# Kernel optimization log

Hardware: AMD Instinct MI355X
Metric: run time of the kernel (lower is better)

## Reference

```python
import jax, jax.numpy as jnp
import numpy as np

# Axial permutations for num_dimensions=3, emb_dim=-1 (total rank 5), att_dims=[1,2,3]
PERMS = [[0, 2, 3, 1, 4], [0, 1, 3, 2, 4], [0, 1, 2, 3, 4]]
H_SELF = 8
H_CROSS = 8
E_HEAD = 64  # dims_embed[0] / (num_heads_self + num_heads_cross) = 1024/16


def layernorm(x, eps=1e-5):
    # nn.LayerNorm(elementwise_affine=False)
    m = x.mean(axis=-1, keepdims=True)
    v = x.var(axis=-1, keepdims=True)
    return (x - m) * jax.lax.rsqrt(v + eps)


def cross_attention(x, kv, wq, wkv, h, e):
    # x: [bb, t, d_q], kv: [bb, t_kv, d_kv]
    q = x @ wq                                   # [bb, t, h*e]
    k, v = jnp.split(kv @ wkv, 2, axis=-1)       # each [bb, t_kv, h*e]
    bb, t = q.shape[0], q.shape[1]
    tk = k.shape[1]
    q = q.reshape(bb, t, h, e)
    k = k.reshape(bb, tk, h, e)
    v = v.reshape(bb, tk, h, e)
    dots = jnp.einsum('bihe,bjhe->bhij', q, k) * (e ** -0.5)
    attn = jax.nn.softmax(dots, axis=-1)
    out = jnp.einsum('bhij,bjhe->bihe', attn, v)
    return out.reshape(bb, t, h * e)


def permute_to_from(x, kv, perm, wq, wkv, h, e):
    inv = list(np.argsort(perm))
    ax = jnp.transpose(x, perm)
    axkv = jnp.transpose(kv, perm)
    shape = list(ax.shape)
    shape_kv = list(axkv.shape)
    t, d = shape[-2], shape[-1]
    t_kv, d_kv = shape_kv[-2], shape_kv[-1]
    r1 = shape[1] / shape_kv[1]
    r2 = shape[2] / shape_kv[2]
    if int(r1) != 1:
        axkv = jnp.repeat(axkv, max(1, int(r1)), axis=1)
        ax = jnp.repeat(ax, max(1, int(1.0 / r1)), axis=1)
    if int(r2) != 1:
        axkv = jnp.repeat(axkv, max(1, int(r2)), axis=2)
        ax = jnp.repeat(ax, max(1, int(1.0 / r2)), axis=2)
    assert ax.shape[1:3] == axkv.shape[1:3]
    perm_shape = list(ax.shape)
    out = cross_attention(ax.reshape(-1, t, d), axkv.reshape(-1, t_kv, d_kv), wq, wkv, h, e)
    out = out.reshape(perm_shape[:-1] + [-1])
    if shape[1] < shape_kv[1]:  # field0 coarser along perm dim 1 -> mean-pool back
        out = out.reshape(shape[:2] + [int(1.0 / r1)] + perm_shape[2:-1] + [-1]).mean(axis=2)
    if shape[2] < shape_kv[2]:
        out = out.reshape(shape[:3] + [int(1.0 / r2)] + perm_shape[3:-1] + [-1]).mean(axis=3)
    out = out.reshape(shape[:-1] + [-1])
    return jnp.transpose(out, inv)


def setup_inputs() -> dict:
    key = jax.random.key(0)
    ks = jax.random.split(key, 8)
    B, T, LA, LO, D0, D1 = 32, 12, 12, 12, 1024, 512
    s = 0.02
    return {
        'x0': jax.random.normal(ks[0], (B, T, LA, LO, D0), dtype=jnp.float32),
        'x1': jax.random.normal(ks[1], (B, T, LA // 2, LO // 2, D1), dtype=jnp.float32),
        'wq_self': jax.random.normal(ks[2], (3, D0, 512), dtype=jnp.float32) * s,
        'wkv_self': jax.random.normal(ks[3], (3, D0, 1024), dtype=jnp.float32) * s,
        'wq_cross': jax.random.normal(ks[4], (3, D0, 512), dtype=jnp.float32) * s,
        'wkv_cross': jax.random.normal(ks[5], (3, D1, 1024), dtype=jnp.float32) * s,
        'w_out': jax.random.normal(ks[6], (3, 1024, D0), dtype=jnp.float32) * s,
        'b_out': jnp.zeros((3, D0), dtype=jnp.float32),
    }


def reference(x0, x1, wq_self, wkv_self, wq_cross, wkv_cross, w_out, b_out):
    pass_through = x0
    f0 = layernorm(x0)
    f1 = layernorm(x1)
    for ip, perm in enumerate(PERMS):
        o_self = permute_to_from(f0, f0, perm, wq_self[ip], wkv_self[ip], H_SELF, E_HEAD)
        o_cross = permute_to_from(f0, f1, perm, wq_cross[ip], wkv_cross[ip], H_CROSS, E_HEAD)
        f0 = jnp.concatenate([o_self, o_cross], axis=-1) @ w_out[ip] + b_out[ip]
    return pass_through + f0
```

## Files before the change

### kernel.cpp

```cpp
#include <hip/hip_runtime.h>
#include <hip/hip_bf16.h>


typedef __bf16 bf16x8 __attribute__((ext_vector_type(8)));
typedef float floatx4 __attribute__((ext_vector_type(4)));

#define N0 55296
#define N1 13824

#define RAW_BARRIER() asm volatile("s_barrier" ::: "memory")
#define VMCNT(n) asm volatile("s_waitcnt vmcnt(" #n ")" ::: "memory")
#define SCHED_FENCE() __builtin_amdgcn_sched_barrier(0)

__device__ __forceinline__ void gload16(const void* g, void* l) {
    __builtin_amdgcn_global_load_lds(
        (const __attribute__((address_space(1))) unsigned int*)g,
        (__attribute__((address_space(3))) unsigned int*)l, 16, 0, 0);
}

template <int SIG>
__device__ __forceinline__ int mapRow(int i) {
    if (SIG == 0) return i;
    const int b = i / 1728, r = i % 1728;
    const int d1 = r / 144, r2 = r % 144, d2 = r2 / 12, d3 = r2 % 12;
    if (SIG == 1) return b * 1728 + d3 * 144 + d1 * 12 + d2;
    if (SIG == 2) return b * 1728 + d3 * 144 + d2 * 12 + d1;
    return b * 1728 + d1 * 144 + d3 * 12 + d2;
}

template <int D>
__device__ __forceinline__ void ln_body(const float* __restrict__ xr,
                                        __hip_bfloat16* __restrict__ yr)
{
    constexpr int V = D / 256;
    const int tid = threadIdx.x;
    float vals[V];
    if constexpr (V == 4) {
        const float4 t4 = *(const float4*)(xr + tid * 4);
        vals[0] = t4.x; vals[1] = t4.y; vals[2] = t4.z; vals[3] = t4.w;
    } else {
        const float2 t2 = *(const float2*)(xr + tid * 2);
        vals[0] = t2.x; vals[1] = t2.y;
    }
    float s = 0.f, q = 0.f;
#pragma unroll
    for (int k = 0; k < V; ++k) { s += vals[k]; q += vals[k] * vals[k]; }
#pragma unroll
    for (int off = 32; off > 0; off >>= 1) {
        s += __shfl_xor(s, off);
        q += __shfl_xor(q, off);
    }
    __shared__ float rs[4], rq[4];
    const int w = tid >> 6;
    if ((tid & 63) == 0) { rs[w] = s; rq[w] = q; }
    __syncthreads();
    s = rs[0] + rs[1] + rs[2] + rs[3];
    q = rq[0] + rq[1] + rq[2] + rq[3];
    const float mean = s * (1.f / D);
    const float var  = q * (1.f / D) - mean * mean;
    const float rstd = rsqrtf(var + 1e-5f);
    __hip_bfloat16 o[V];
#pragma unroll
    for (int k = 0; k < V; ++k) o[k] = __float2bfloat16((vals[k] - mean) * rstd);
    if constexpr (V == 4) *(uint2*)(yr + tid * 4) = *(const uint2*)o;
    else                  *(uint*)(yr + tid * 2)  = *(const uint*)o;
}

__global__ __launch_bounds__(256)
void ln_all(const float* __restrict__ x0, const float* __restrict__ x1,
            __hip_bfloat16* __restrict__ f0, __hip_bfloat16* __restrict__ f1)
{
    const int row = blockIdx.x;
    if (row < N0) {
        ln_body<1024>(x0 + (size_t)row * 1024, f0 + (size_t)row * 1024);
    } else {
        const int r = row - N0;
        ln_body<512>(x1 + (size_t)r * 512, f1 + (size_t)r * 512);
    }
}

__global__ __launch_bounds__(256)
void transpose_all(const float* __restrict__ wqs, const float* __restrict__ wkvs,
                   const float* __restrict__ wqc, const float* __restrict__ wkvc,
                   const float* __restrict__ wo,
                   __hip_bfloat16* __restrict__ W1t,
                   __hip_bfloat16* __restrict__ W2t,
                   __hip_bfloat16* __restrict__ W3t,
                   __hip_bfloat16* __restrict__ W3o)
{
    int idx = blockIdx.x;
    if (idx >= 8704) {
        const size_t i = ((size_t)(idx - 8704) * 256 + threadIdx.x) * 4;
        const float4 v = *(const float4*)(wo + i);
        __hip_bfloat16 o[4] = { __float2bfloat16(v.x), __float2bfloat16(v.y),
                                __float2bfloat16(v.z), __float2bfloat16(v.w) };
        *(uint2*)(W3o + i) = *(const uint2*)o;
        return;
    }
    const float* src;
    __hip_bfloat16* dst;
    int K, N;
    if (idx < 1536) {
        const int ip = idx / 512; idx %= 512; K = 1024; N = 512;
        src = wqs + (size_t)ip * 524288;  dst = W1t + (size_t)ip * 2097152;
    } else if (idx < 4608) {
        idx -= 1536;
        const int ip = idx / 1024; idx %= 1024; K = 1024; N = 1024;
        src = wkvs + (size_t)ip * 1048576; dst = W1t + (size_t)ip * 2097152 + 524288;
    } else if (idx < 6144) {
        idx -= 4608;
        const int ip = idx / 512; idx %= 512; K = 1024; N = 512;
        src = wqc + (size_t)ip * 524288;  dst = W1t + (size_t)ip * 2097152 + 1572864;
    } else if (idx < 7680) {
        idx -= 6144;
        const int ip = idx / 512; idx %= 512; K = 512; N = 1024;
        src = wkvc + (size_t)ip * 524288; dst = W2t + (size_t)ip * 524288;
    } else {
        idx -= 7680;
        K = 1024; N = 1024;
        src = wo + (size_t)2 * 1048576;  dst = W3t + (size_t)2 * 1048576;
    }
    const int tiles_x = N >> 5;
    const int n0 = (idx % tiles_x) * 32, k0 = (idx / tiles_x) * 32;

    __shared__ float tile[32][33];
    const int tx = threadIdx.x & 31, ty = threadIdx.x >> 5;
#pragma unroll
    for (int d = 0; d < 4; ++d)
        tile[ty + d * 8][tx] = src[(size_t)(k0 + ty + d * 8) * N + n0 + tx];
    __syncthreads();
#pragma unroll
    for (int d = 0; d < 4; ++d)
        dst[(size_t)(n0 + ty + d * 8) * K + k0 + tx] = __float2bfloat16(tile[tx][ty + d * 8]);
}

__global__ __launch_bounds__(256)
void bfold_kernel(const float* __restrict__ b_out,
                  const __hip_bfloat16* __restrict__ W1t,
                  float* __restrict__ bf)
{
    const int idx = blockIdx.x * 256 + threadIdx.x;
    const int j = idx >> 11, n = idx & 2047;
    const float* b = b_out + j * 1024;
    const __hip_bfloat16* w = W1t + ((size_t)(j + 1) * 2048 + n) * 1024;
    float s = 0.f;
#pragma unroll 4
    for (int d = 0; d < 1024; ++d) s += b[d] * __bfloat162float(w[d]);
    bf[idx] = s;
}

template <int EPI, int SIG>
__global__ __launch_bounds__(512)
void gemm8p(const __hip_bfloat16* __restrict__ A,
            const __hip_bfloat16* __restrict__ Bt,
            void* __restrict__ Cv,
            const float* __restrict__ bias,
            const float* __restrict__ resid,
            int M, int N, int K, int lda,
            size_t zsA, size_t zsB, size_t zsC)
{
    __shared__ __align__(16) char lds[131072];

    A  += (size_t)blockIdx.z * zsA;
    Bt += (size_t)blockIdx.z * zsB;
    Cv = (void*)((__hip_bfloat16*)Cv + (size_t)blockIdx.z * zsC);

    const int gx  = gridDim.x;
    const int nwg = gx * gridDim.y;
    const int bid = blockIdx.y * gx + blockIdx.x;
    const int swz = (bid & 7) * (nwg >> 3) + (bid >> 3);
    const int m0 = (swz / gx) * 256;
    const int n0 = (swz % gx) * 256;

    const int t    = threadIdx.x;
    const int w    = t >> 6;
    const int lane = t & 63;
    const int wr   = w >> 2;
    const int wc   = w & 3;
    const int fr   = lane & 15;
    const int ksl  = lane >> 4;

    floatx4 acc[8][4] = {};

    const int tr   = t >> 3;
    const int scol = ((t & 7) ^ (tr & 7)) << 3;
    const __hip_bfloat16* aP[4];
#pragma unroll
    for (int r = 0; r < 4; ++r)
        aP[r] = A + (size_t)mapRow<SIG>(m0 + tr + r * 64) * lda + scol;
    const __hip_bfloat16* bG = Bt + (size_t)(n0 + ((tr >> 5) * 64) + (tr & 31)) * K + scol;
    const int ldst = t * 16;

    const int cg0 = ksl ^ (fr & 7);
    const int aO0 = (wr * 64 + fr) * 128 + cg0 * 16;
    const int bO0 = (wc * 32 + fr) * 128 + cg0 * 16;

    auto stageA = [&](char* buf, int h, int ka) {
        gload16(aP[h]     + ka, buf + h * 16384 + ldst);
        gload16(aP[h + 2] + ka, buf + h * 16384 + 8192 + ldst);
    };
    auto stageB = [&](char* buf, int h, int kb) {
        gload16(bG + kb + (size_t)(h * 32)       * K, buf + 32768 + h * 16384 + ldst);
        gload16(bG + kb + (size_t)(h * 32 + 128) * K, buf + 32768 + h * 16384 + 8192 + ldst);
    };

    const char* bufC = lds;
    auto ldA = [&](int h, bf16x8 (&a)[2][4]) {
#pragma unroll
        for (int mm = 0; mm < 4; ++mm) {
            a[0][mm] = *(const bf16x8*)(bufC + h * 16384 + mm * 2048 + aO0);
            a[1][mm] = *(const bf16x8*)(bufC + h * 16384 + mm * 2048 + (aO0 ^ 64));
        }
    };
    auto ldB = [&](int h, bf16x8 (&b)[2][2]) {
#pragma unroll
        for (int nn = 0; nn < 2; ++nn) {
            b[0][nn] = *(const bf16x8*)(bufC + 32768 + h * 16384 + nn * 2048 + bO0);
            b[1][nn] = *(const bf16x8*)(bufC + 32768 + h * 16384 + nn * 2048 + (bO0 ^ 64));
        }
    };
    auto quad = [&](bf16x8 (&a)[2][4], bf16x8 (&b)[2][2], int mlo, int nlo) {
        __builtin_amdgcn_s_setprio(1);
#pragma unroll
        for (int kk = 0; kk < 2; ++kk)
#pragma unroll
            for (int mm = 0; mm < 4; ++mm)
#pragma unroll
                for (int nn = 0; nn < 2; ++nn)
                    acc[mlo + mm][nlo + nn] = __builtin_amdgcn_mfma_f32_16x16x32_bf16(
                        a[kk][mm], b[kk][nn], acc[mlo + mm][nlo + nn], 0, 0, 0);
        __builtin_amdgcn_s_setprio(0);
    };

    const int NT = K >> 6;

    stageA(lds, 0, 0);
    stageB(lds, 0, 0);
    stageA(lds, 1, 0);
    stageB(lds, 1, 0);
    VMCNT(4);
    RAW_BARRIER();

    bf16x8 a0[2][4], a1[2][4], b0[2][2], b1[2][2];
    ldA(0, a0);

    for (int tt = 0; tt < NT - 1; ++tt) {
        bufC = lds + ((tt & 1) << 16);
        char* bufN = lds + (((tt + 1) & 1) << 16);
        const int kc = (tt + 1) << 6;
        ldB(0, b0);
        stageA(bufN, 0, kc);
        SCHED_FENCE();
        quad(a0, b0, 0, 0);
        VMCNT(4); RAW_BARRIER();
        ldA(1, a1);
        stageB(bufN, 0, kc);
        SCHED_FENCE();
        quad(a1, b0, 4, 0);
        VMCNT(4); RAW_BARRIER();
        ldB(1, b1);
        stageA(bufN, 1, kc);
        SCHED_FENCE();
        quad(a0, b1, 0, 2);
        VMCNT(4); RAW_BARRIER();
        bufC = bufN;
        ldA(0, a0);
        stageB(bufN, 1, kc);
        SCHED_FENCE();
        quad(a1, b1, 4, 2);
        VMCNT(4); RAW_BARRIER();
    }

    bufC = lds + (((NT - 1) & 1) << 16);
    ldB(0, b0);
    SCHED_FENCE();
    quad(a0, b0, 0, 0);
    VMCNT(2); RAW_BARRIER();
    ldA(1, a1);
    SCHED_FENCE();
    quad(a1, b0, 4, 0);
    VMCNT(0); RAW_BARRIER();
    ldB(1, b1);
    SCHED_FENCE();
    quad(a0, b1, 0, 2);
    quad(a1, b1, 4, 2);

#pragma unroll
    for (int m = 0; m < 8; ++m) {
#pragma unroll
        for (int n = 0; n < 4; ++n) {
            const int col = n0 + wc * 64 + n * 16 + fr;
#pragma unroll
            for (int r = 0; r < 4; ++r) {
                const int row = m0 + wr * 128 + m * 16 + ksl * 4 + r;
                const size_t idx = (size_t)row * N + col;
                const float v = acc[m][n][r];
                if (EPI == 0) {
                    ((__hip_bfloat16*)Cv)[idx] = __float2bfloat16(v);
                } else if (EPI == 1) {
                    ((__hip_bfloat16*)Cv)[idx] = __float2bfloat16(v + bias[col]);
                } else {
                    ((float*)Cv)[idx] = resid[idx] + v + bias[col];
                }
            }
        }
    }
}

__global__ __launch_bounds__(512)
void attn_fused(const __hip_bfloat16* __restrict__ qkv,
                const __hip_bfloat16* __restrict__ kvc,
                __hip_bfloat16* __restrict__ out, int ip)
{
    __shared__ __align__(16) __hip_bfloat16 R[12][2056];
    __shared__ __align__(16) __hip_bfloat16 KV[12][1032];
    __shared__ __hip_bfloat16 P[16][12][12];

    const int g   = blockIdx.x;
    const int tid = threadIdx.x;

    const int b  = g / 144;
    const int u1 = (g / 12) % 12;
    const int u2 = g % 12;
    int kvb, kvstride, tkc;
    if (ip == 0) {
        kvb = b * 432 + (u1 >> 1) * 6 + (u2 >> 1); kvstride = 36; tkc = 12;
    } else if (ip == 1) {
        kvb = b * 432 + u1 * 36 + (u2 >> 1); kvstride = 6; tkc = 6;
    } else {
        kvb = b * 432 + u1 * 36 + (u2 >> 1) * 6; kvstride = 1; tkc = 6;
    }

    const uint4* src = (const uint4*)(qkv + (size_t)g * 12 * 2048);
    for (int idx = tid; idx < 12 * 256; idx += 512) {
        const int row = idx >> 8, cg = idx & 255;
        *(uint4*)(&R[row][cg * 8]) = src[row * 256 + cg];
    }
    for (int idx = tid; idx < tkc * 128; idx += 512) {
        const int row = idx >> 7, cg = idx & 127;
        const uint4* kvr = (const uint4*)(kvc + (size_t)(kvb + row * kvstride) * 3072);
        *(uint4*)(&KV[row][cg * 8]) = kvr[cg];
    }
    __syncthreads();

    const int nd_self = 8 * 12 * 12;
    const int nd = nd_self + 8 * 12 * tkc;
    for (int idx = tid; idx < nd; idx += 512) {
        int h, i, j;
        const bf16x8 *q8, *k8;
        const bool self = idx < nd_self;
        if (self) {
            h = idx / 144; const int rem = idx % 144; i = rem / 12; j = rem % 12;
            q8 = (const bf16x8*)(&R[i][h * 64]);
            k8 = (const bf16x8*)(&R[j][512 + h * 64]);
        } else {
            const int x = idx - nd_self;
            h = x / (12 * tkc); const int rem = x % (12 * tkc); i = rem / tkc; j = rem % tkc;
            q8 = (const bf16x8*)(&R[i][1536 + h * 64]);
            k8 = (const bf16x8*)(&KV[j][h * 64]);
        }
        float s = 0.f;
#pragma unroll
        for (int e = 0; e < 8; ++e) {
            const bf16x8 qv = q8[e];
            const bf16x8 kv = k8[e];
#pragma unroll
            for (int x2 = 0; x2 < 8; ++x2)
                s += (float)qv[x2] * (float)kv[x2];
        }
        P[self ? h : 8 + h][i][j] = __float2bfloat16(s * 0.125f);
    }
    __syncthreads();

    if (tid < 192) {
        const int half = tid / 96, h = (tid % 96) / 12, i = tid % 12;
        const int tk = half ? tkc : 12;
        __hip_bfloat16* p = &P[half * 8 + h][i][0];
        float v[12];
        float mx = -1e30f;
        for (int j = 0; j < tk; ++j) { v[j] = __bfloat162float(p[j]); mx = fmaxf(mx, v[j]); }
        float sum = 0.f;
        for (int j = 0; j < tk; ++j) { v[j] = __expf(v[j] - mx); sum += v[j]; }
        const float inv = 1.f / sum;
        for (int j = 0; j < tk; ++j) p[j] = __float2bfloat16(v[j] * inv);
    }
    __syncthreads();

    for (int idx = tid; idx < 12 * 128; idx += 512) {
        const int i = idx >> 7, g8 = idx & 127;
        float acc8[8] = {};
        int colbase;
        if (g8 < 64) {
            const int h = g8 >> 3;
            colbase = g8 * 8;
#pragma unroll
            for (int j = 0; j < 12; ++j) {
                const float p = __bfloat162float(P[h][i][j]);
                const bf16x8 v = *(const bf16x8*)(&R[j][1024 + g8 * 8]);
#pragma unroll
                for (int e = 0; e < 8; ++e) acc8[e] += p * (float)v[e];
            }
        } else {
            const int cc = g8 - 64;
            const int h = cc >> 3;
            colbase = 512 + cc * 8;
            for (int j = 0; j < tkc; ++j) {
                const float p = __bfloat162float(P[8 + h][i][j]);
                const bf16x8 v = *(const bf16x8*)(&KV[j][512 + cc * 8]);
#pragma unroll
                for (int e = 0; e < 8; ++e) acc8[e] += p * (float)v[e];
            }
        }
        __hip_bfloat16 o[8];
#pragma unroll
        for (int e = 0; e < 8; ++e) o[e] = __float2bfloat16(acc8[e]);
        *(uint4*)(out + (size_t)(g * 12 + i) * 1024 + colbase) = *(const uint4*)o;
    }
}

extern "C" void kernel_launch(void* const* d_in, const int* in_sizes, int n_in,
                              void* d_out, int out_size, void* d_ws, size_t ws_size,
                              hipStream_t stream)
{
    (void)in_sizes; (void)n_in; (void)out_size; (void)ws_size;
    const float* x0        = (const float*)d_in[0];
    const float* x1        = (const float*)d_in[1];
    const float* wq_self   = (const float*)d_in[2];
    const float* wkv_self  = (const float*)d_in[3];
    const float* wq_cross  = (const float*)d_in[4];
    const float* wkv_cross = (const float*)d_in[5];
    const float* w_out     = (const float*)d_in[6];
    const float* b_out     = (const float*)d_in[7];

    __hip_bfloat16* qkv = (__hip_bfloat16*)d_out;

    char* ws = (char*)d_ws;
    size_t off = 0;
    auto alloc = [&](size_t bytes) {
        void* p = ws + off;
        off += (bytes + 255) & ~(size_t)255;
        return p;
    };
    __hip_bfloat16* f0   = (__hip_bfloat16*)alloc((size_t)N0 * 1024 * 2);
    __hip_bfloat16* f1   = (__hip_bfloat16*)alloc((size_t)N1 * 512 * 2);
    __hip_bfloat16* kvc3 = (__hip_bfloat16*)alloc((size_t)N1 * 3072 * 2);
    __hip_bfloat16* W1t  = (__hip_bfloat16*)alloc((size_t)3 * 2048 * 1024 * 2);
    __hip_bfloat16* W2t  = (__hip_bfloat16*)alloc((size_t)3 * 1024 * 512 * 2);
    __hip_bfloat16* W3t  = (__hip_bfloat16*)alloc((size_t)3 * 1024 * 1024 * 2);
    __hip_bfloat16* W3o  = (__hip_bfloat16*)alloc((size_t)2 * 1024 * 1024 * 2);
    __hip_bfloat16* Wf   = (__hip_bfloat16*)alloc((size_t)2 * 2048 * 1024 * 2);
    float*          bfo  = (float*)alloc((size_t)2 * 2048 * 4);

    ln_all<<<N0 + N1, 256, 0, stream>>>(x0, x1, f0, f1);
    transpose_all<<<10752, 256, 0, stream>>>(wq_self, wkv_self, wq_cross,
                                             wkv_cross, w_out, W1t, W2t, W3t, W3o);
    bfold_kernel<<<16, 256, 0, stream>>>(b_out, W1t, bfo);
    gemm8p<0, 0><<<dim3(4, 8, 2), 512, 0, stream>>>(
        W1t + (size_t)2048 * 1024, W3o, Wf, nullptr, nullptr,
        2048, 1024, 1024, 1024,
        (size_t)2048 * 1024, (size_t)1024 * 1024, (size_t)2048 * 1024);
    gemm8p<0, 0><<<dim3(12, 54), 512, 0, stream>>>(
        f1, W2t, kvc3, nullptr, nullptr, N1, 3072, 512, 512, 0, 0, 0);

    gemm8p<0, 1><<<dim3(8, 216), 512, 0, stream>>>(
        f0, W1t, qkv, nullptr, nullptr, N0, 2048, 1024, 1024, 0, 0, 0);
    attn_fused<<<4608, 512, 0, stream>>>(qkv, kvc3, f0, 0);

    gemm8p<1, 2><<<dim3(8, 216), 512, 0, stream>>>(
        f0, Wf, qkv, bfo, nullptr, N0, 2048, 1024, 1024, 0, 0, 0);
    attn_fused<<<4608, 512, 0, stream>>>(qkv, kvc3 + 1024, f0, 1);

    gemm8p<1, 3><<<dim3(8, 216), 512, 0, stream>>>(
        f0, Wf + (size_t)2048 * 1024, qkv, bfo + 2048, nullptr, N0, 2048, 1024, 1024, 0, 0, 0);
    attn_fused<<<4608, 512, 0, stream>>>(qkv, kvc3 + 2048, f0, 2);

    gemm8p<2, 0><<<dim3(4, 216), 512, 0, stream>>>(
        f0, W3t + (size_t)2 * 1024 * 1024, d_out, b_out + 2 * 1024, x0,
        N0, 1024, 1024, 1024, 0, 0, 0);
}
```

Measured before the change: 1.452 ms.

## Replace double-buffered pipelined GEMM main loop with single-buffer synchronous loop

Removes the two-buffer software pipeline that overlapped global-to-LDS loads for the next K tile with MFMA work on the current one. Each iteration now loads the whole tile, waits for all loads to finish, computes, then waits on LDS reads before the next iteration. This halves shared memory to 64KB, which could allow more resident workgroups, but it exposes global memory latency on every K step.

```diff
diff --git a/kernel.cpp b/kernel.cpp
--- a/kernel.cpp
+++ b/kernel.cpp
@@ -10,7 +10,7 @@
 
 #define RAW_BARRIER() asm volatile("s_barrier" ::: "memory")
 #define VMCNT(n) asm volatile("s_waitcnt vmcnt(" #n ")" ::: "memory")
-#define SCHED_FENCE() __builtin_amdgcn_sched_barrier(0)
+#define LGKMCNT0() asm volatile("s_waitcnt lgkmcnt(0)" ::: "memory")
 
 __device__ __forceinline__ void gload16(const void* g, void* l) {
     __builtin_amdgcn_global_load_lds(
@@ -159,7 +159,7 @@
             int M, int N, int K, int lda,
             size_t zsA, size_t zsB, size_t zsC)
 {
-    __shared__ __align__(16) char lds[131072];
+    __shared__ __align__(16) char lds[65536];
 
     A  += (size_t)blockIdx.z * zsA;
     Bt += (size_t)blockIdx.z * zsB;
@@ -195,28 +195,27 @@
     const int aO0 = (wr * 64 + fr) * 128 + cg0 * 16;
     const int bO0 = (wc * 32 + fr) * 128 + cg0 * 16;
 
-    auto stageA = [&](char* buf, int h, int ka) {
-        gload16(aP[h]     + ka, buf + h * 16384 + ldst);
-        gload16(aP[h + 2] + ka, buf + h * 16384 + 8192 + ldst);
-    };
-    auto stageB = [&](char* buf, int h, int kb) {
-        gload16(bG + kb + (size_t)(h * 32)       * K, buf + 32768 + h * 16384 + ldst);
-        gload16(bG + kb + (size_t)(h * 32 + 128) * K, buf + 32768 + h * 16384 + 8192 + ldst);
-    };
-
-    const char* bufC = lds;
+    auto stageA = [&](int h, int ka) {
+        gload16(aP[h]     + ka, lds + h * 16384 + ldst);
+        gload16(aP[h + 2] + ka, lds + h * 16384 + 8192 + ldst);
+    };
+    auto stageB = [&](int h, int kb) {
+        gload16(bG + kb + (size_t)(h * 32)       * K, lds + 32768 + h * 16384 + ldst);
+        gload16(bG + kb + (size_t)(h * 32 + 128) * K, lds + 32768 + h * 16384 + 8192 + ldst);
+    };
+
     auto ldA = [&](int h, bf16x8 (&a)[2][4]) {
 #pragma unroll
         for (int mm = 0; mm < 4; ++mm) {
-            a[0][mm] = *(const bf16x8*)(bufC + h * 16384 + mm * 2048 + aO0);
-            a[1][mm] = *(const bf16x8*)(bufC + h * 16384 + mm * 2048 + (aO0 ^ 64));
+            a[0][mm] = *(const bf16x8*)(lds + h * 16384 + mm * 2048 + aO0);
+            a[1][mm] = *(const bf16x8*)(lds + h * 16384 + mm * 2048 + (aO0 ^ 64));
         }
     };
     auto ldB = [&](int h, bf16x8 (&b)[2][2]) {
 #pragma unroll
         for (int nn = 0; nn < 2; ++nn) {
-            b[0][nn] = *(const bf16x8*)(bufC + 32768 + h * 16384 + nn * 2048 + bO0);
-            b[1][nn] = *(const bf16x8*)(bufC + 32768 + h * 16384 + nn * 2048 + (bO0 ^ 64));
+            b[0][nn] = *(const bf16x8*)(lds + 32768 + h * 16384 + nn * 2048 + bO0);
+            b[1][nn] = *(const bf16x8*)(lds + 32768 + h * 16384 + nn * 2048 + (bO0 ^ 64));
         }
     };
     auto quad = [&](bf16x8 (&a)[2][4], bf16x8 (&b)[2][2], int mlo, int nlo) {
@@ -233,57 +232,25 @@
     };
 
     const int NT = K >> 6;
-
-    stageA(lds, 0, 0);
-    stageB(lds, 0, 0);
-    stageA(lds, 1, 0);
-    stageB(lds, 1, 0);
-    VMCNT(4);
-    RAW_BARRIER();
-
     bf16x8 a0[2][4], a1[2][4], b0[2][2], b1[2][2];
-    ldA(0, a0);
-
-    for (int tt = 0; tt < NT - 1; ++tt) {
-        bufC = lds + ((tt & 1) << 16);
-        char* bufN = lds + (((tt + 1) & 1) << 16);
-        const int kc = (tt + 1) << 6;
-        ldB(0, b0);
-        stageA(bufN, 0, kc);
-        SCHED_FENCE();
+
+    for (int tt = 0; tt < NT; ++tt) {
+        const int kc = tt << 6;
+        stageA(0, kc);
+        stageB(0, kc);
+        stageA(1, kc);
+        stageB(1, kc);
+        VMCNT(0); RAW_BARRIER();
+        ldA(0, a0); ldB(0, b0);
         quad(a0, b0, 0, 0);
-        VMCNT(4); RAW_BARRIER();
         ldA(1, a1);
-        stageB(bufN, 0, kc);
-        SCHED_FENCE();
         quad(a1, b0, 4, 0);
-        VMCNT(4); RAW_BARRIER();
         ldB(1, b1);
-        stageA(bufN, 1, kc);
-        SCHED_FENCE();
         quad(a0, b1, 0, 2);
-        VMCNT(4); RAW_BARRIER();
-        bufC = bufN;
-        ldA(0, a0);
-        stageB(bufN, 1, kc);
-        SCHED_FENCE();
         quad(a1, b1, 4, 2);
-        VMCNT(4); RAW_BARRIER();
-    }
-
-    bufC = lds + (((NT - 1) & 1) << 16);
-    ldB(0, b0);
-    SCHED_FENCE();
-    quad(a0, b0, 0, 0);
-    VMCNT(2); RAW_BARRIER();
-    ldA(1, a1);
-    SCHED_FENCE();
-    quad(a1, b0, 4, 0);
-    VMCNT(0); RAW_BARRIER();
-    ldB(1, b1);
-    SCHED_FENCE();
-    quad(a0, b1, 0, 2);
-    quad(a1, b1, 4, 2);
+        LGKMCNT0();
+        RAW_BARRIER();
+    }
 
 #pragma unroll
     for (int m = 0; m < 8; ++m) {
```

New measurement: 1.890 ms. +30.2%, slower.
